# Kernel optimization log

Measured on AMD Instinct MI355X. Metric: run time of the kernel, lower is better.

The kernel has to match this reference:

```python
import jax, jax.numpy as jnp
import numpy as np

# dims: B batch, T timesteps, V nodes, D in-features, C channels, d pos-emb dim,
# TS = t_size (spatio-temporal window), P prediction steps, L layers (=4, fixed by GLU(C*4))
B, T, V, D, C, d, TS, P, L = 4, 12, 512, 1, 64, 8, 3, 12, 4
BETA = TS - 1


def setup_inputs() -> dict:
    key = jax.random.key(0)
    ks = jax.random.split(key, 30)
    n = lambda i, shape, s=1.0: jax.random.normal(ks[i], shape, dtype=jnp.float32) * s
    return dict(
        x=n(0, (B, T, V, D)),
        sape=n(1, (V, d)),
        tape=n(2, (B, T, 1, d)),
        srpe=n(3, (V, V, d)),
        trpe=n(4, (TS, 1, d)),
        zeros_x=jnp.zeros((B, BETA, V, C), jnp.float32),
        zeros_tape=jnp.zeros((B, BETA, 1, d), jnp.float32),
        range_mask=(jax.random.uniform(ks[5], (B, V, TS * V)) < 0.5).astype(jnp.float32),
        Wi=n(6, (D, C), D ** -0.5), bi=n(7, (C,), 0.02),
        gc_mu=n(8, (L, 6, d)), gc_sig=n(9, (L, 6, d), 0.5),
        Wg=n(10, (L, C, 2 * C), C ** -0.5), bg=n(11, (L, 2 * C), 0.02),
        Wsp=n(12, (L, d, 2 * C), d ** -0.5), Wtp=n(13, (L, d, 2 * C), d ** -0.5),
        fs_w=n(14, (L, C, C, T), (C * T) ** -0.5), fs_b=n(15, (L, C), 0.02),
        glu1_w=n(16, (L, 2 * C, C), C ** -0.5), glu1_b=n(17, (L, 2 * C), 0.02),
        gout_w=n(18, (8 * C, 4 * C), (4 * C) ** -0.5), gout_b=n(19, (8 * C,), 0.02),
        out_w=n(20, (P, 4 * C), (4 * C) ** -0.5), out_b=n(21, (P,), 0.02),
    )


def _glu_cv(w, b, y):
    # 1x1-conv GLU over channel dim of y: (B, Cin, V) -> (B, Cin, V)
    z = jnp.einsum('oc,bcv->bov', w, y) + b[None, :, None]
    zl, zr = jnp.split(z, 2, axis=1)
    return zl * jax.nn.sigmoid(zr)


def _forward(x, sape, tape, srpe, trpe, Wi, bi, gc_mu, gc_sig, Wg, bg, Wsp, Wtp,
             fs_w, fs_b, glu1_w, glu1_b, gout_w, gout_b, out_w, out_b,
             zeros_x, zeros_tape, range_mask):
    b_, t_ = x.shape[0], x.shape[1]
    v_ = sape.shape[0]
    ts = trpe.shape[0]
    widx = jnp.arange(t_)[:, None] + jnp.arange(ts)  # (T, t_size) sliding-window indices
    h = x @ Wi + bi                                   # InputLayer: B,T,V,C
    tape_pad = jnp.concatenate([zeros_tape, tape], axis=1)  # B,T+beta,1,d
    skips = []
    for l in range(gc_mu.shape[0]):
        mu, sig = gc_mu[l], gc_sig[l]
        gc = lambda emb, i: jnp.sum(-0.5 * (emb - mu[i]) ** 2 * sig[i] ** 2, axis=-1)
        # STPRI: Gaussian position-aware relation inference
        base = gc(sape, 0)[:, None] + gc(sape, 1)[None, :] + gc(srpe, 4)        # (V_i, V_j)
        per_t = gc(tape, 2)[:, :, 0][:, :, None] \
              + gc(tape_pad, 3)[:, :, 0][:, widx] \
              + gc(trpe, 5)[:, 0]                                               # B,T,t_size
        S = jnp.exp(per_t[:, :, :, None, None] + base)                          # B,T,k,i,j (<=1, safe)
        S = S.transpose(0, 1, 4, 2, 3).reshape(b_, t_, v_, ts * v_)             # B,T,j,(k*V+i)
        S = S * range_mask[:, None]                                             # masked relations
        # STPGConv: masked graph conv over the t_size*V window + gating
        x_pad = jnp.concatenate([zeros_x, h], axis=1)                           # B,T+beta,V,C
        xw = x_pad[:, widx].reshape(b_, t_, ts * v_, -1)                        # B,T,t_size*V,C
        g = jnp.einsum('btjm,btmc->btjc', S, xw) @ Wg[l] + bg[l]                # B,T,V,2C
        g = g + sape @ Wsp[l] + tape @ Wtp[l]                                   # +SE(V,2C) +TE(B,T,1,2C)
        gl, gr = jnp.split(g, 2, axis=-1)
        h = gl * jax.nn.sigmoid(gr)                                             # B,T,V,C
        # GFS: conv over time (kernel (1,T)) + GLU -> B,C,V
        y = jnp.einsum('bcvt,oct->bov', h.transpose(0, 3, 2, 1), fs_w[l]) + fs_b[l][None, :, None]
        skips.append(_glu_cv(glu1_w[l], glu1_b[l], y))
    s = _glu_cv(gout_w, gout_b, jnp.concatenate(skips, axis=1))                  # B,4C,V
    return jnp.einsum('oc,bcv->bov', out_w, s) + out_b[None, :, None]            # B,P,V


def reference(x, sape, tape, srpe, trpe, zeros_x, zeros_tape, range_mask, Wi, bi,
              gc_mu, gc_sig, Wg, bg, Wsp, Wtp, fs_w, fs_b, glu1_w, glu1_b,
              gout_w, gout_b, out_w, out_b):
    return _forward(x, sape, tape, srpe, trpe, Wi, bi, gc_mu, gc_sig, Wg, bg, Wsp, Wtp,
                    fs_w, fs_b, glu1_w, glu1_b, gout_w, gout_b, out_w, out_b,
                    zeros_x, zeros_tape, range_mask)
```

## Files before the change

kernel.cpp:

```cpp
#include <hip/hip_runtime.h>
#include <math.h>


typedef unsigned short u16;
typedef __attribute__((ext_vector_type(8))) short short8;
typedef __attribute__((ext_vector_type(4))) float f32x4;
typedef __attribute__((ext_vector_type(8))) unsigned short u16x8;
typedef __attribute__((ext_vector_type(4))) unsigned short u16x4;

#define MFMA16(a, b, c) __builtin_amdgcn_mfma_f32_16x16x32_bf16((a), (b), (c), 0, 0, 0)

__device__ __forceinline__ float b2f(u16 u) {
  union { unsigned int i; float f; } x; x.i = ((unsigned int)u) << 16; return x.f;
}
__device__ __forceinline__ u16 f2b(float f) {
  union { float f; unsigned int i; } x; x.f = f;
  unsigned int r = x.i + 0x7FFFu + ((x.i >> 16) & 1u);
  return (u16)(r >> 16);
}
__device__ __forceinline__ void ld8f(const float* __restrict__ p, float* f) {
  f32x4 a = *(const f32x4*)p;
  f32x4 b = *(const f32x4*)(p + 4);
  #pragma unroll
  for (int i = 0; i < 4; ++i) { f[i] = a[i]; f[4 + i] = b[i]; }
}
__device__ __forceinline__ float gcf(const float* e, const float* __restrict__ mu,
                                     const float* __restrict__ sg) {
  float s = 0.f;
  #pragma unroll
  for (int i = 0; i < 8; ++i) {
    float dm = e[i] - mu[i];
    s += dm * dm * sg[i] * sg[i];
  }
  return -0.5f * s;
}
__device__ __forceinline__ float sigm(float v) { return 1.0f / (1.0f + expf(-v)); }

__global__ __launch_bounds__(256) void prep_kernel(
    const float* __restrict__ x, const float* __restrict__ sape,
    const float* __restrict__ tape, const float* __restrict__ srpe,
    const float* __restrict__ trpe, const float* __restrict__ Wi,
    const float* __restrict__ bi, const float* __restrict__ gmu,
    const float* __restrict__ gsg, const float* __restrict__ Wg,
    const float* __restrict__ bg, const float* __restrict__ Wsp,
    const float* __restrict__ Wtp, const float* __restrict__ fsw,
    const float* __restrict__ mask,
    const float* __restrict__ g1w, const float* __restrict__ gw,
    const float* __restrict__ ow,
    u16* __restrict__ hT0, u16* __restrict__ Abf,
    float* __restrict__ spb, float* __restrict__ tpb,
    u16* __restrict__ fswT, u16* __restrict__ WgT, float* __restrict__ ev,
    u16* __restrict__ g1wB, u16* __restrict__ gwB, u16* __restrict__ owB) {
  const int tid = threadIdx.x;
  int bid = blockIdx.x;

  if (bid < 768) {
    int gid = bid * 256 + tid;
    int i8 = gid & 63, c = (gid >> 6) & 63, bt = gid >> 12;
    float xv[8];
    ld8f(&x[bt * 512 + i8 * 8], xv);
    float wic = Wi[c], bic = bi[c];
    u16x8 hv;
    #pragma unroll
    for (int ii = 0; ii < 8; ++ii) hv[ii] = f2b(xv[ii] * wic + bic);
    *(u16x8*)&hT0[gid * 8] = hv;
    return;
  }
  bid -= 768;
  if (bid < 1024) {
    int gid = bid * 256 + tid;
    int i = gid & 511, j = gid >> 9;
    float fi[8], fj[8], fr[8];
    ld8f(sape + i * 8, fi);
    ld8f(sape + j * 8, fj);
    ld8f(srpe + ((size_t)i * 512 + j) * 8, fr);
    u16 eb[4];
    #pragma unroll
    for (int l = 0; l < 4; ++l) {
      const float* mub = gmu + l * 48;
      const float* sgb = gsg + l * 48;
      float s = gcf(fi, mub + 0, sgb + 0)
              + gcf(fj, mub + 8, sgb + 8)
              + gcf(fr, mub + 32, sgb + 32);
      eb[l] = f2b(expf(s));
    }
    #pragma unroll
    for (int b = 0; b < 4; ++b)
      #pragma unroll
      for (int k = 0; k < 3; ++k) {
        float mv = mask[((size_t)(b * 512 + j)) * 1536 + k * 512 + i];
        u16 m = (mv != 0.f) ? (u16)0xFFFFu : (u16)0;
        #pragma unroll
        for (int l = 0; l < 4; ++l)
          Abf[((size_t)((l * 4 + b) * 512 + j)) * 1536 + k * 512 + i] = eb[l] & m;
      }
    return;
  }
  bid -= 1024;
  if (bid < 1024) {
    int gid = bid * 256 + tid;
    int o = gid & 127, j = (gid >> 7) & 511, l = gid >> 16;
    float a = 0.f;
    #pragma unroll
    for (int dd = 0; dd < 8; ++dd)
      a += sape[j * 8 + dd] * Wsp[(l * 8 + dd) * 128 + o];
    spb[gid] = a;
    return;
  }
  bid -= 1024;
  if (bid < 96) {
    int gid = bid * 256 + tid;
    int o = gid & 127, bt = (gid >> 7) % 48, l = gid / 6144;
    float a = bg[l * 128 + o];
    #pragma unroll
    for (int dd = 0; dd < 8; ++dd)
      a += tape[bt * 8 + dd] * Wtp[(l * 8 + dd) * 128 + o];
    tpb[gid] = a;
    return;
  }
  bid -= 96;
  if (bid < 768) {
    int gid = bid * 256 + tid;
    int kidx = gid % 768, rest = gid / 768;
    int o = rest & 63, l = rest >> 6;
    int c = kidx & 63, tt = kidx >> 6;
    fswT[gid] = f2b(fsw[((l * 64 + o) * 64 + c) * 12 + tt]);
    return;
  }
  bid -= 768;
  if (bid < 128) {
    int gid = bid * 256 + tid;
    int c = gid & 63, o = (gid >> 6) & 127, l = gid >> 13;
    WgT[gid] = f2b(Wg[(l * 64 + c) * 128 + o]);
    return;
  }
  bid -= 128;
  if (bid < 3) {
    int gid = bid * 256 + tid;
    if (gid < 576) {
      int k = gid % 3, t = (gid / 3) % 12, b = (gid / 36) % 4, l = gid / 144;
      const float* mub = gmu + l * 48;
      const float* sgb = gsg + l * 48;
      float e2[8], e3[8], e5[8];
      ld8f(tape + (b * 12 + t) * 8, e2);
      int tp = t + k - 2;
      if (tp >= 0) ld8f(tape + (b * 12 + tp) * 8, e3);
      else {
        #pragma unroll
        for (int ii = 0; ii < 8; ++ii) e3[ii] = 0.f;
      }
      ld8f(trpe + k * 8, e5);
      float s = gcf(e2, mub + 16, sgb + 16)
              + gcf(e3, mub + 24, sgb + 24)
              + gcf(e5, mub + 40, sgb + 40);
      ev[gid] = expf(s);
    }
    return;
  }
  bid -= 3;
  if (bid < 128) {
    int gid = bid * 256 + tid;
    g1wB[gid] = f2b(g1w[gid]);
    return;
  }
  bid -= 128;
  if (bid < 512) {
    int gid = bid * 256 + tid;
    gwB[gid] = f2b(gw[gid]);
    return;
  }
  bid -= 512;
  {
    int gid = bid * 256 + tid;
    if (gid < 3072) owB[gid] = f2b(ow[gid]);
  }
}

__global__ __launch_bounds__(256) void agg_kernel(
    const u16* __restrict__ Abfl, const u16* __restrict__ hT,
    u16* __restrict__ G) {
  __shared__ u16 As[128][72];
  __shared__ u16 Bs[128][72];
  const int tid = threadIdx.x, wid = tid >> 6, lane = tid & 63;
  const int l16 = lane & 15, quad = lane >> 4;
  const int bid = blockIdx.x;
  const int nt = bid % 6;
  const int mt = (bid / 6) & 3;
  const int k  = (bid / 24) % 3;
  const int b  = bid / 72;
  const int wm = wid >> 1, wn = wid & 1;

  const u16* Arow0 = Abfl + ((size_t)(b * 512 + mt * 128)) * 1536 + k * 512;
  f32x4 acc[4][4] = {};

  for (int it = 0; it < 8; ++it) {
    const int i0 = it * 64;
    #pragma unroll
    for (int s = 0; s < 4; ++s) {
      int idx = s * 256 + tid;
      int r = idx >> 3, ch = (idx & 7) * 8;
      *(u16x8*)&As[r][ch] = *(const u16x8*)&Arow0[(size_t)r * 1536 + i0 + ch];
      int tp = nt * 2 + (r >> 6), c = r & 63;
      *(u16x8*)&Bs[r][ch] =
          *(const u16x8*)&hT[((size_t)((b * 12 + tp) * 64 + c)) * 512 + i0 + ch];
    }
    __syncthreads();
    #pragma unroll
    for (int ks = 0; ks < 2; ++ks) {
      short8 af[4], bf[4];
      #pragma unroll
      for (int mb = 0; mb < 4; ++mb)
        af[mb] = *(const short8*)&As[wm * 64 + mb * 16 + l16][ks * 32 + quad * 8];
      #pragma unroll
      for (int nb = 0; nb < 4; ++nb)
        bf[nb] = *(const short8*)&Bs[wn * 64 + nb * 16 + l16][ks * 32 + quad * 8];
      #pragma unroll
      for (int mb = 0; mb < 4; ++mb)
        #pragma unroll
        for (int nb = 0; nb < 4; ++nb)
          acc[mb][nb] = MFMA16(af[mb], bf[nb], acc[mb][nb]);
    }
    __syncthreads();
  }

  u16* Gp = G + ((size_t)((b * 3 + k) * 512 + mt * 128)) * 768 + nt * 128;
  #pragma unroll
  for (int mb = 0; mb < 4; ++mb)
    #pragma unroll
    for (int nb = 0; nb < 4; ++nb) {
      int n = wn * 64 + nb * 16 + l16;
      #pragma unroll
      for (int r = 0; r < 4; ++r) {
        int m = wm * 64 + mb * 16 + quad * 4 + r;
        Gp[(size_t)m * 768 + n] = f2b(acc[mb][nb][r]);
      }
    }
}

__global__ __launch_bounds__(256) void combine_kernel(
    const u16* __restrict__ G, const float* __restrict__ evl,
    const u16* __restrict__ WgTl, const float* __restrict__ spbl,
    const float* __restrict__ tpbl, const u16* __restrict__ fswTl,
    u16* __restrict__ hTout, float* __restrict__ yptl) {
  __shared__ u16 aggL[128][72];
  __shared__ u16 hL[128][72];
  const int tid = threadIdx.x, wid = tid >> 6, lane = tid & 63;
  const int l16 = lane & 15, quad = lane >> 4;
  const int bid = blockIdx.x;
  const int mt = bid & 3;
  const int bt = bid >> 2;
  const int b = bt / 12, t = bt - b * 12;

  {
    int j = tid >> 1;
    int c0 = (tid & 1) * 32;
    float accv[32];
    #pragma unroll
    for (int ii = 0; ii < 32; ++ii) accv[ii] = 0.f;
    #pragma unroll
    for (int k = 0; k < 3; ++k) {
      int tp = t + k - 2;
      if (tp < 0) continue;
      float ek = evl[bt * 3 + k];
      const u16* gp = &G[((size_t)((b * 3 + k) * 512 + mt * 128 + j)) * 768 + tp * 64 + c0];
      #pragma unroll
      for (int s = 0; s < 4; ++s) {
        u16x8 gv = *(const u16x8*)&gp[s * 8];
        #pragma unroll
        for (int ii = 0; ii < 8; ++ii) accv[s * 8 + ii] += b2f(gv[ii]) * ek;
      }
    }
    #pragma unroll
    for (int s = 0; s < 4; ++s) {
      u16x8 ov;
      #pragma unroll
      for (int ii = 0; ii < 8; ++ii) ov[ii] = f2b(accv[s * 8 + ii]);
      *(u16x8*)&aggL[j][c0 + s * 8] = ov;
    }
  }
  __syncthreads();

  f32x4 acc2[8][2] = {};
  #pragma unroll
  for (int ks = 0; ks < 2; ++ks) {
    short8 bf[2];
    #pragma unroll
    for (int nb = 0; nb < 2; ++nb)
      bf[nb] = *(const short8*)&aggL[wid * 32 + nb * 16 + l16][ks * 32 + quad * 8];
    #pragma unroll
    for (int mb = 0; mb < 8; ++mb) {
      short8 a = *(const short8*)&WgTl[(mb * 16 + l16) * 64 + ks * 32 + quad * 8];
      acc2[mb][0] = MFMA16(a, bf[0], acc2[mb][0]);
      acc2[mb][1] = MFMA16(a, bf[1], acc2[mb][1]);
    }
  }

  #pragma unroll
  for (int mb = 0; mb < 4; ++mb) {
    int ob = mb * 16 + quad * 4;
    #pragma unroll
    for (int nb = 0; nb < 2; ++nb) {
      int jl = wid * 32 + nb * 16 + l16;
      int jg = mt * 128 + jl;
      f32x4 spl = *(const f32x4*)&spbl[jg * 128 + ob];
      f32x4 spr = *(const f32x4*)&spbl[jg * 128 + 64 + ob];
      f32x4 tpl = *(const f32x4*)&tpbl[bt * 128 + ob];
      f32x4 tpr = *(const f32x4*)&tpbl[bt * 128 + 64 + ob];
      #pragma unroll
      for (int r = 0; r < 4; ++r) {
        float vl = acc2[mb][nb][r] + spl[r] + tpl[r];
        float vr = acc2[mb + 4][nb][r] + spr[r] + tpr[r];
        u16 hb = f2b(vl * sigm(vr));
        hTout[((size_t)((b * 12 + t) * 64 + ob + r)) * 512 + jg] = hb;
        hL[jl][ob + r] = hb;
      }
    }
  }
  __syncthreads();

  f32x4 accY[4][2] = {};
  #pragma unroll
  for (int ks = 0; ks < 2; ++ks) {
    short8 bfv[2];
    #pragma unroll
    for (int nb = 0; nb < 2; ++nb)
      bfv[nb] = *(const short8*)&hL[wid * 32 + nb * 16 + l16][ks * 32 + quad * 8];
    #pragma unroll
    for (int mb = 0; mb < 4; ++mb) {
      short8 a = *(const short8*)&fswTl[(mb * 16 + l16) * 768 + t * 64 + ks * 32 + quad * 8];
      accY[mb][0] = MFMA16(a, bfv[0], accY[mb][0]);
      accY[mb][1] = MFMA16(a, bfv[1], accY[mb][1]);
    }
  }
  #pragma unroll
  for (int mb = 0; mb < 4; ++mb)
    #pragma unroll
    for (int nb = 0; nb < 2; ++nb) {
      int j = mt * 128 + wid * 32 + nb * 16 + l16;
      #pragma unroll
      for (int r = 0; r < 4; ++r) {
        int o = mb * 16 + quad * 4 + r;
        yptl[((size_t)(bt * 64 + o)) * 512 + j] = accY[mb][nb][r];
      }
    }
}

__global__ __launch_bounds__(256) void reduce_kernel(
    const float* __restrict__ ypt, const float* __restrict__ fsb,
    u16* __restrict__ yB) {
  int gid = blockIdx.x * 256 + threadIdx.x;
  int j4 = gid & 127, o = (gid >> 7) & 63, b = (gid >> 13) & 3, l = gid >> 15;
  const float* base = &ypt[(size_t)l * 1572864 +
                           ((size_t)((b * 12) * 64 + o)) * 512 + j4 * 4];
  float fb = fsb[l * 64 + o];
  f32x4 s = {fb, fb, fb, fb};
  #pragma unroll
  for (int t = 0; t < 12; ++t) s += *(const f32x4*)&base[(size_t)t * 32768];
  u16x4 pk;
  #pragma unroll
  for (int ii = 0; ii < 4; ++ii) pk[ii] = f2b(s[ii]);
  *(u16x4*)&yB[((size_t)((l * 4 + b) * 64 + o)) * 512 + j4 * 4] = pk;
}

__global__ __launch_bounds__(256) void final_kernel(
    const u16* __restrict__ yB,
    const u16* __restrict__ g1wB, const float* __restrict__ g1b,
    const u16* __restrict__ gwB, const float* __restrict__ gb,
    const u16* __restrict__ owB, const float* __restrict__ obv,
    float* __restrict__ out) {
  __shared__ u16 yL[64][72];
  __shared__ float zL[128][72];
  __shared__ u16 cL[64][264];
  __shared__ u16 sT[64][264];
  const int tid = threadIdx.x, wid = tid >> 6, lane = tid & 63;
  const int l16 = lane & 15, quad = lane >> 4;
  const int b = blockIdx.x >> 3;
  const int v0 = (blockIdx.x & 7) * 64;

  for (int l = 0; l < 4; ++l) {
    {
      int o = tid & 63, sv = tid >> 6;
      const u16* src = &yB[((size_t)((l * 4 + b) * 64 + o)) * 512 + v0 + sv * 16];
      u16x8 p0 = *(const u16x8*)&src[0];
      u16x8 p1 = *(const u16x8*)&src[8];
      #pragma unroll
      for (int ii = 0; ii < 8; ++ii) {
        yL[sv * 16 + ii][o] = p0[ii];
        yL[sv * 16 + 8 + ii][o] = p1[ii];
      }
    }
    __syncthreads();
    f32x4 a1[2][4] = {};
    #pragma unroll
    for (int ks = 0; ks < 2; ++ks) {
      short8 bfv[4];
      #pragma unroll
      for (int nb = 0; nb < 4; ++nb)
        bfv[nb] = *(const short8*)&yL[nb * 16 + l16][ks * 32 + quad * 8];
      #pragma unroll
      for (int mb = 0; mb < 2; ++mb) {
        short8 a = *(const short8*)&g1wB[l * 8192 + (wid * 32 + mb * 16 + l16) * 64 +
                                         ks * 32 + quad * 8];
        #pragma unroll
        for (int nb = 0; nb < 4; ++nb) a1[mb][nb] = MFMA16(a, bfv[nb], a1[mb][nb]);
      }
    }
    #pragma unroll
    for (int mb = 0; mb < 2; ++mb)
      #pragma unroll
      for (int nb = 0; nb < 4; ++nb)
        #pragma unroll
        for (int r = 0; r < 4; ++r)
          zL[wid * 32 + mb * 16 + quad * 4 + r][nb * 16 + l16] = a1[mb][nb][r];
    __syncthreads();
    {
      int o = tid >> 2, vv0 = (tid & 3) * 16;
      float bl = g1b[l * 128 + o], br = g1b[l * 128 + 64 + o];
      #pragma unroll
      for (int ii = 0; ii < 16; ++ii) {
        float zl = zL[o][vv0 + ii] + bl;
        float zr = zL[o + 64][vv0 + ii] + br;
        cL[vv0 + ii][l * 64 + o] = f2b(zl * sigm(zr));
      }
    }
    __syncthreads();
  }

  f32x4 acc[8][4] = {};
  #pragma unroll
  for (int ks = 0; ks < 8; ++ks) {
    short8 bf[4];
    #pragma unroll
    for (int nb = 0; nb < 4; ++nb)
      bf[nb] = *(const short8*)&cL[nb * 16 + l16][ks * 32 + quad * 8];
    #pragma unroll
    for (int mb = 0; mb < 8; ++mb) {
      int og = (mb < 4 ? wid * 64 + mb * 16 : 256 + wid * 64 + (mb - 4) * 16) + l16;
      short8 a = *(const short8*)&gwB[og * 256 + ks * 32 + quad * 8];
      #pragma unroll
      for (int nb = 0; nb < 4; ++nb) acc[mb][nb] = MFMA16(a, bf[nb], acc[mb][nb]);
    }
  }
  #pragma unroll
  for (int mb = 0; mb < 4; ++mb)
    #pragma unroll
    for (int nb = 0; nb < 4; ++nb) {
      int vloc = nb * 16 + l16;
      int cc0 = wid * 64 + mb * 16 + quad * 4;
      u16x4 pk;
      #pragma unroll
      for (int r = 0; r < 4; ++r) {
        float zl = acc[mb][nb][r] + gb[cc0 + r];
        float zr = acc[mb + 4][nb][r] + gb[256 + cc0 + r];
        pk[r] = f2b(zl * sigm(zr));
      }
      *(u16x4*)&sT[vloc][cc0] = pk;
    }
  __syncthreads();

  f32x4 acc3 = {};
  #pragma unroll
  for (int ks = 0; ks < 8; ++ks) {
    short8 a;
    if (l16 < 12) a = *(const short8*)&owB[l16 * 256 + ks * 32 + quad * 8];
    else {
      #pragma unroll
      for (int ii = 0; ii < 8; ++ii) a[ii] = 0;
    }
    short8 bf = *(const short8*)&sT[wid * 16 + l16][ks * 32 + quad * 8];
    acc3 = MFMA16(a, bf, acc3);
  }
  #pragma unroll
  for (int r = 0; r < 4; ++r) {
    int p = quad * 4 + r;
    if (p < 12)
      out[(b * 12 + p) * 512 + v0 + wid * 16 + l16] = acc3[r] + obv[p];
  }
}

extern "C" void kernel_launch(void* const* d_in, const int* in_sizes, int n_in,
                              void* d_out, int out_size, void* d_ws, size_t ws_size,
                              hipStream_t stream) {
  const float* x    = (const float*)d_in[0];
  const float* sape = (const float*)d_in[1];
  const float* tape = (const float*)d_in[2];
  const float* srpe = (const float*)d_in[3];
  const float* trpe = (const float*)d_in[4];
  const float* mask = (const float*)d_in[7];
  const float* Wi   = (const float*)d_in[8];
  const float* bi   = (const float*)d_in[9];
  const float* gmu  = (const float*)d_in[10];
  const float* gsg  = (const float*)d_in[11];
  const float* Wg   = (const float*)d_in[12];
  const float* bg   = (const float*)d_in[13];
  const float* Wsp  = (const float*)d_in[14];
  const float* Wtp  = (const float*)d_in[15];
  const float* fsw  = (const float*)d_in[16];
  const float* fsb  = (const float*)d_in[17];
  const float* g1w  = (const float*)d_in[18];
  const float* g1b  = (const float*)d_in[19];
  const float* gow  = (const float*)d_in[20];
  const float* gob  = (const float*)d_in[21];
  const float* ow   = (const float*)d_in[22];
  const float* obv  = (const float*)d_in[23];

  char* w = (char*)d_ws;
  u16*   hT_a = (u16*)(w + 0);
  u16*   hT_b = (u16*)(w + 3145728);
  u16*   Abf  = (u16*)(w + 6291456);
  u16*   G    = (u16*)(w + 31457280);
  u16*   fswT = (u16*)(w + 40894464);
  u16*   WgT  = (u16*)(w + 41287680);
  u16*   g1wB = (u16*)(w + 41353216);
  u16*   gwB  = (u16*)(w + 41418752);
  u16*   owB  = (u16*)(w + 41680896);
  float* spb  = (float*)(w + 41689088);
  float* tpb  = (float*)(w + 42737664);
  float* ev   = (float*)(w + 42835968);
  float* ypt  = (float*)(w + 42852352);
  u16*   yB   = (u16*)(w + 68018176);

  prep_kernel<<<4463, 256, 0, stream>>>(x, sape, tape, srpe, trpe, Wi, bi, gmu, gsg,
                                        Wg, bg, Wsp, Wtp, fsw, mask, g1w, gow, ow,
                                        hT_a, Abf, spb, tpb, fswT, WgT, ev,
                                        g1wB, gwB, owB);
  u16* hin = hT_a;
  u16* hout = hT_b;
  for (int l = 0; l < 4; ++l) {
    agg_kernel<<<288, 256, 0, stream>>>(Abf + (size_t)l * 3145728, hin, G);
    combine_kernel<<<192, 256, 0, stream>>>(G, ev + l * 144, WgT + l * 8192,
                                            spb + l * 65536, tpb + l * 6144,
                                            fswT + l * 49152, hout,
                                            ypt + (size_t)l * 1572864);
    u16* tmp = hin; hin = hout; hout = tmp;
  }
  reduce_kernel<<<512, 256, 0, stream>>>(ypt, fsb, yB);
  final_kernel<<<32, 256, 0, stream>>>(yB, g1wB, g1b, gwB, gob, owB, obv,
                                       (float*)d_out);
}
```

Baseline: 266.1 us.

## Fuse aggregation GEMM with combine/GLU/time-conv into a single per-layer kernel

Merges agg_kernel and combine_kernel into one layer_kernel. Each block computes the three window-offset aggregations for two timesteps, mixes them with the edge weights in registers, and then runs the Wg GEMM, GLU and fs-conv partial products. This removes the bf16 G intermediate round trip and one launch per layer. The fs partial sums are also pre-reduced over timestep pairs, which halves the ypt buffer that reduce_kernel reads. In exchange each block holds more accumulators (3x2x4 tiles), uses a smaller M tile, and skips work for negative timesteps, which leaves the load across blocks uneven.

```diff
diff --git a/kernel.cpp b/kernel.cpp
--- a/kernel.cpp
+++ b/kernel.cpp
@@ -176,190 +176,160 @@
   }
 }
 
-__global__ __launch_bounds__(256) void agg_kernel(
-    const u16* __restrict__ Abfl, const u16* __restrict__ hT,
-    u16* __restrict__ G) {
-  __shared__ u16 As[128][72];
+__global__ __launch_bounds__(256) void layer_kernel(
+    const u16* __restrict__ Abfl, const u16* __restrict__ hTin,
+    const float* __restrict__ evl, const u16* __restrict__ WgTl,
+    const float* __restrict__ spbl, const float* __restrict__ tpbl,
+    const u16* __restrict__ fswTl, u16* __restrict__ hTout,
+    float* __restrict__ ypnl) {
+  __shared__ u16 As[64][72];
   __shared__ u16 Bs[128][72];
+  __shared__ u16 Cs[2][64][72];
+  __shared__ u16 hL[64][72];
   const int tid = threadIdx.x, wid = tid >> 6, lane = tid & 63;
   const int l16 = lane & 15, quad = lane >> 4;
+  const int wm = wid >> 1, wn = wid & 1;
   const int bid = blockIdx.x;
   const int nt = bid % 6;
-  const int mt = (bid / 6) & 3;
-  const int k  = (bid / 24) % 3;
-  const int b  = bid / 72;
-  const int wm = wid >> 1, wn = wid & 1;
-
-  const u16* Arow0 = Abfl + ((size_t)(b * 512 + mt * 128)) * 1536 + k * 512;
-  f32x4 acc[4][4] = {};
-
-  for (int it = 0; it < 8; ++it) {
-    const int i0 = it * 64;
-    #pragma unroll
-    for (int s = 0; s < 4; ++s) {
-      int idx = s * 256 + tid;
-      int r = idx >> 3, ch = (idx & 7) * 8;
-      *(u16x8*)&As[r][ch] = *(const u16x8*)&Arow0[(size_t)r * 1536 + i0 + ch];
-      int tp = nt * 2 + (r >> 6), c = r & 63;
-      *(u16x8*)&Bs[r][ch] =
-          *(const u16x8*)&hT[((size_t)((b * 12 + tp) * 64 + c)) * 512 + i0 + ch];
+  const int mt = (bid / 6) & 7;
+  const int b  = bid / 48;
+
+  const int r0 = tid >> 3, ch0 = (tid & 7) * 8;
+  f32x4 acc[3][2][4] = {};
+
+  for (int k = 0; k < 3; ++k) {
+    const int tp0 = 2 * nt + k - 2;
+    if (tp0 + 1 < 0) continue;
+    for (int it = 0; it < 8; ++it) {
+      const int i0 = it * 64;
+      #pragma unroll
+      for (int s = 0; s < 2; ++s) {
+        int r = r0 + s * 32;
+        *(u16x8*)&As[r][ch0] =
+            *(const u16x8*)&Abfl[(size_t)(b * 512 + mt * 64 + r) * 1536 + k * 512 + i0 + ch0];
+      }
+      #pragma unroll
+      for (int s = 0; s < 4; ++s) {
+        int r = r0 + s * 32;
+        int tsel = r >> 6, c = r & 63;
+        int tp = tp0 + tsel;
+        u16x8 v;
+        if (tp >= 0)
+          v = *(const u16x8*)&hTin[((size_t)((b * 12 + tp) * 64 + c)) * 512 + i0 + ch0];
+        else {
+          #pragma unroll
+          for (int ii = 0; ii < 8; ++ii) v[ii] = 0;
+        }
+        *(u16x8*)&Bs[r][ch0] = v;
+      }
+      __syncthreads();
+      #pragma unroll
+      for (int ks = 0; ks < 2; ++ks) {
+        short8 af[2], bf[4];
+        #pragma unroll
+        for (int mb = 0; mb < 2; ++mb)
+          af[mb] = *(const short8*)&As[wm * 32 + mb * 16 + l16][ks * 32 + quad * 8];
+        #pragma unroll
+        for (int nb = 0; nb < 4; ++nb)
+          bf[nb] = *(const short8*)&Bs[wn * 64 + nb * 16 + l16][ks * 32 + quad * 8];
+        #pragma unroll
+        for (int mb = 0; mb < 2; ++mb)
+          #pragma unroll
+          for (int nb = 0; nb < 4; ++nb)
+            acc[k][mb][nb] = MFMA16(af[mb], bf[nb], acc[k][mb][nb]);
+      }
+      __syncthreads();
+    }
+  }
+
+  {
+    const int t_w = 2 * nt + wn;
+    const float e0 = evl[(b * 12 + t_w) * 3 + 0];
+    const float e1 = evl[(b * 12 + t_w) * 3 + 1];
+    const float e2 = evl[(b * 12 + t_w) * 3 + 2];
+    #pragma unroll
+    for (int mb = 0; mb < 2; ++mb)
+      #pragma unroll
+      for (int nb = 0; nb < 4; ++nb)
+        #pragma unroll
+        for (int r = 0; r < 4; ++r) {
+          float cv = e0 * acc[0][mb][nb][r] + e1 * acc[1][mb][nb][r] +
+                     e2 * acc[2][mb][nb][r];
+          Cs[wn][wm * 32 + mb * 16 + quad * 4 + r][nb * 16 + l16] = f2b(cv);
+        }
+  }
+  __syncthreads();
+
+  f32x4 accY[4] = {};
+  for (int tsel = 0; tsel < 2; ++tsel) {
+    const int t = 2 * nt + tsel, bt = b * 12 + t;
+    f32x4 a2[2][4] = {};
+    #pragma unroll
+    for (int ks = 0; ks < 2; ++ks) {
+      short8 bf[4];
+      #pragma unroll
+      for (int nb = 0; nb < 4; ++nb)
+        bf[nb] = *(const short8*)&Cs[tsel][nb * 16 + l16][ks * 32 + quad * 8];
+      #pragma unroll
+      for (int mb = 0; mb < 2; ++mb) {
+        short8 a = *(const short8*)&WgTl[(mb * 64 + wid * 16 + l16) * 64 +
+                                         ks * 32 + quad * 8];
+        #pragma unroll
+        for (int nb = 0; nb < 4; ++nb) a2[mb][nb] = MFMA16(a, bf[nb], a2[mb][nb]);
+      }
+    }
+    #pragma unroll
+    for (int nb = 0; nb < 4; ++nb) {
+      int jg = mt * 64 + nb * 16 + l16;
+      #pragma unroll
+      for (int r = 0; r < 4; ++r) {
+        int o = wid * 16 + quad * 4 + r;
+        float vl = a2[0][nb][r] + spbl[jg * 128 + o] + tpbl[bt * 128 + o];
+        float vr = a2[1][nb][r] + spbl[jg * 128 + 64 + o] + tpbl[bt * 128 + 64 + o];
+        u16 hb = f2b(vl * sigm(vr));
+        hTout[((size_t)(bt * 64 + o)) * 512 + jg] = hb;
+        hL[nb * 16 + l16][o] = hb;
+      }
     }
     __syncthreads();
     #pragma unroll
     for (int ks = 0; ks < 2; ++ks) {
-      short8 af[4], bf[4];
-      #pragma unroll
-      for (int mb = 0; mb < 4; ++mb)
-        af[mb] = *(const short8*)&As[wm * 64 + mb * 16 + l16][ks * 32 + quad * 8];
-      #pragma unroll
-      for (int nb = 0; nb < 4; ++nb)
-        bf[nb] = *(const short8*)&Bs[wn * 64 + nb * 16 + l16][ks * 32 + quad * 8];
-      #pragma unroll
-      for (int mb = 0; mb < 4; ++mb)
-        #pragma unroll
-        for (int nb = 0; nb < 4; ++nb)
-          acc[mb][nb] = MFMA16(af[mb], bf[nb], acc[mb][nb]);
+      short8 a = *(const short8*)&fswTl[(wid * 16 + l16) * 768 + t * 64 +
+                                        ks * 32 + quad * 8];
+      #pragma unroll
+      for (int nb = 0; nb < 4; ++nb) {
+        short8 bf = *(const short8*)&hL[nb * 16 + l16][ks * 32 + quad * 8];
+        accY[nb] = MFMA16(a, bf, accY[nb]);
+      }
     }
     __syncthreads();
   }
-
-  u16* Gp = G + ((size_t)((b * 3 + k) * 512 + mt * 128)) * 768 + nt * 128;
-  #pragma unroll
-  for (int mb = 0; mb < 4; ++mb)
-    #pragma unroll
-    for (int nb = 0; nb < 4; ++nb) {
-      int n = wn * 64 + nb * 16 + l16;
-      #pragma unroll
-      for (int r = 0; r < 4; ++r) {
-        int m = wm * 64 + mb * 16 + quad * 4 + r;
-        Gp[(size_t)m * 768 + n] = f2b(acc[mb][nb][r]);
-      }
-    }
-}
-
-__global__ __launch_bounds__(256) void combine_kernel(
-    const u16* __restrict__ G, const float* __restrict__ evl,
-    const u16* __restrict__ WgTl, const float* __restrict__ spbl,
-    const float* __restrict__ tpbl, const u16* __restrict__ fswTl,
-    u16* __restrict__ hTout, float* __restrict__ yptl) {
-  __shared__ u16 aggL[128][72];
-  __shared__ u16 hL[128][72];
-  const int tid = threadIdx.x, wid = tid >> 6, lane = tid & 63;
-  const int l16 = lane & 15, quad = lane >> 4;
-  const int bid = blockIdx.x;
-  const int mt = bid & 3;
-  const int bt = bid >> 2;
-  const int b = bt / 12, t = bt - b * 12;
-
-  {
-    int j = tid >> 1;
-    int c0 = (tid & 1) * 32;
-    float accv[32];
-    #pragma unroll
-    for (int ii = 0; ii < 32; ++ii) accv[ii] = 0.f;
-    #pragma unroll
-    for (int k = 0; k < 3; ++k) {
-      int tp = t + k - 2;
-      if (tp < 0) continue;
-      float ek = evl[bt * 3 + k];
-      const u16* gp = &G[((size_t)((b * 3 + k) * 512 + mt * 128 + j)) * 768 + tp * 64 + c0];
-      #pragma unroll
-      for (int s = 0; s < 4; ++s) {
-        u16x8 gv = *(const u16x8*)&gp[s * 8];
-        #pragma unroll
-        for (int ii = 0; ii < 8; ++ii) accv[s * 8 + ii] += b2f(gv[ii]) * ek;
-      }
-    }
-    #pragma unroll
-    for (int s = 0; s < 4; ++s) {
-      u16x8 ov;
-      #pragma unroll
-      for (int ii = 0; ii < 8; ++ii) ov[ii] = f2b(accv[s * 8 + ii]);
-      *(u16x8*)&aggL[j][c0 + s * 8] = ov;
-    }
-  }
-  __syncthreads();
-
-  f32x4 acc2[8][2] = {};
-  #pragma unroll
-  for (int ks = 0; ks < 2; ++ks) {
-    short8 bf[2];
-    #pragma unroll
-    for (int nb = 0; nb < 2; ++nb)
-      bf[nb] = *(const short8*)&aggL[wid * 32 + nb * 16 + l16][ks * 32 + quad * 8];
-    #pragma unroll
-    for (int mb = 0; mb < 8; ++mb) {
-      short8 a = *(const short8*)&WgTl[(mb * 16 + l16) * 64 + ks * 32 + quad * 8];
-      acc2[mb][0] = MFMA16(a, bf[0], acc2[mb][0]);
-      acc2[mb][1] = MFMA16(a, bf[1], acc2[mb][1]);
-    }
-  }
-
-  #pragma unroll
-  for (int mb = 0; mb < 4; ++mb) {
-    int ob = mb * 16 + quad * 4;
-    #pragma unroll
-    for (int nb = 0; nb < 2; ++nb) {
-      int jl = wid * 32 + nb * 16 + l16;
-      int jg = mt * 128 + jl;
-      f32x4 spl = *(const f32x4*)&spbl[jg * 128 + ob];
-      f32x4 spr = *(const f32x4*)&spbl[jg * 128 + 64 + ob];
-      f32x4 tpl = *(const f32x4*)&tpbl[bt * 128 + ob];
-      f32x4 tpr = *(const f32x4*)&tpbl[bt * 128 + 64 + ob];
-      #pragma unroll
-      for (int r = 0; r < 4; ++r) {
-        float vl = acc2[mb][nb][r] + spl[r] + tpl[r];
-        float vr = acc2[mb + 4][nb][r] + spr[r] + tpr[r];
-        u16 hb = f2b(vl * sigm(vr));
-        hTout[((size_t)((b * 12 + t) * 64 + ob + r)) * 512 + jg] = hb;
-        hL[jl][ob + r] = hb;
-      }
-    }
-  }
-  __syncthreads();
-
-  f32x4 accY[4][2] = {};
-  #pragma unroll
-  for (int ks = 0; ks < 2; ++ks) {
-    short8 bfv[2];
-    #pragma unroll
-    for (int nb = 0; nb < 2; ++nb)
-      bfv[nb] = *(const short8*)&hL[wid * 32 + nb * 16 + l16][ks * 32 + quad * 8];
-    #pragma unroll
-    for (int mb = 0; mb < 4; ++mb) {
-      short8 a = *(const short8*)&fswTl[(mb * 16 + l16) * 768 + t * 64 + ks * 32 + quad * 8];
-      accY[mb][0] = MFMA16(a, bfv[0], accY[mb][0]);
-      accY[mb][1] = MFMA16(a, bfv[1], accY[mb][1]);
-    }
-  }
-  #pragma unroll
-  for (int mb = 0; mb < 4; ++mb)
-    #pragma unroll
-    for (int nb = 0; nb < 2; ++nb) {
-      int j = mt * 128 + wid * 32 + nb * 16 + l16;
-      #pragma unroll
-      for (int r = 0; r < 4; ++r) {
-        int o = mb * 16 + quad * 4 + r;
-        yptl[((size_t)(bt * 64 + o)) * 512 + j] = accY[mb][nb][r];
-      }
-    }
+  #pragma unroll
+  for (int nb = 0; nb < 4; ++nb) {
+    int jg = mt * 64 + nb * 16 + l16;
+    #pragma unroll
+    for (int r = 0; r < 4; ++r) {
+      int o2 = wid * 16 + quad * 4 + r;
+      ypnl[((size_t)(b * 6 + nt)) * 32768 + o2 * 512 + jg] = accY[nb][r];
+    }
+  }
 }
 
 __global__ __launch_bounds__(256) void reduce_kernel(
-    const float* __restrict__ ypt, const float* __restrict__ fsb,
+    const float* __restrict__ ypn, const float* __restrict__ fsb,
     u16* __restrict__ yB) {
   int gid = blockIdx.x * 256 + threadIdx.x;
-  int j4 = gid & 127, o = (gid >> 7) & 63, b = (gid >> 13) & 3, l = gid >> 15;
-  const float* base = &ypt[(size_t)l * 1572864 +
-                           ((size_t)((b * 12) * 64 + o)) * 512 + j4 * 4];
+  int v4 = gid & 127, o = (gid >> 7) & 63, b = (gid >> 13) & 3, l = gid >> 15;
+  const float* base = &ypn[(size_t)l * 786432 + ((size_t)(b * 6)) * 32768 +
+                           o * 512 + v4 * 4];
   float fb = fsb[l * 64 + o];
   f32x4 s = {fb, fb, fb, fb};
   #pragma unroll
-  for (int t = 0; t < 12; ++t) s += *(const f32x4*)&base[(size_t)t * 32768];
+  for (int nt = 0; nt < 6; ++nt) s += *(const f32x4*)&base[(size_t)nt * 32768];
   u16x4 pk;
   #pragma unroll
   for (int ii = 0; ii < 4; ++ii) pk[ii] = f2b(s[ii]);
-  *(u16x4*)&yB[((size_t)((l * 4 + b) * 64 + o)) * 512 + j4 * 4] = pk;
+  *(u16x4*)&yB[((size_t)((l * 4 + b) * 64 + o)) * 512 + v4 * 4] = pk;
 }
 
 __global__ __launch_bounds__(256) void final_kernel(
@@ -508,17 +478,16 @@
   u16*   hT_a = (u16*)(w + 0);
   u16*   hT_b = (u16*)(w + 3145728);
   u16*   Abf  = (u16*)(w + 6291456);
-  u16*   G    = (u16*)(w + 31457280);
-  u16*   fswT = (u16*)(w + 40894464);
-  u16*   WgT  = (u16*)(w + 41287680);
-  u16*   g1wB = (u16*)(w + 41353216);
-  u16*   gwB  = (u16*)(w + 41418752);
-  u16*   owB  = (u16*)(w + 41680896);
-  float* spb  = (float*)(w + 41689088);
-  float* tpb  = (float*)(w + 42737664);
-  float* ev   = (float*)(w + 42835968);
-  float* ypt  = (float*)(w + 42852352);
-  u16*   yB   = (u16*)(w + 68018176);
+  u16*   fswT = (u16*)(w + 31457280);
+  u16*   WgT  = (u16*)(w + 31850496);
+  u16*   g1wB = (u16*)(w + 31916032);
+  u16*   gwB  = (u16*)(w + 31981568);
+  u16*   owB  = (u16*)(w + 32243712);
+  float* spb  = (float*)(w + 32251904);
+  float* tpb  = (float*)(w + 33300480);
+  float* ev   = (float*)(w + 33398784);
+  float* ypn  = (float*)(w + 33415168);
+  u16*   yB   = (u16*)(w + 45998080);
 
   prep_kernel<<<4463, 256, 0, stream>>>(x, sape, tape, srpe, trpe, Wi, bi, gmu, gsg,
                                         Wg, bg, Wsp, Wtp, fsw, mask, g1w, gow, ow,
@@ -527,14 +496,14 @@
   u16* hin = hT_a;
   u16* hout = hT_b;
   for (int l = 0; l < 4; ++l) {
-    agg_kernel<<<288, 256, 0, stream>>>(Abf + (size_t)l * 3145728, hin, G);
-    combine_kernel<<<192, 256, 0, stream>>>(G, ev + l * 144, WgT + l * 8192,
-                                            spb + l * 65536, tpb + l * 6144,
-                                            fswT + l * 49152, hout,
-                                            ypt + (size_t)l * 1572864);
+    layer_kernel<<<192, 256, 0, stream>>>(Abf + (size_t)l * 3145728, hin,
+                                          ev + l * 144, WgT + l * 8192,
+                                          spb + l * 65536, tpb + l * 6144,
+                                          fswT + l * 49152, hout,
+                                          ypn + (size_t)l * 786432);
     u16* tmp = hin; hin = hout; hout = tmp;
   }
-  reduce_kernel<<<512, 256, 0, stream>>>(ypt, fsb, yB);
+  reduce_kernel<<<512, 256, 0, stream>>>(ypn, fsb, yB);
   final_kernel<<<32, 256, 0, stream>>>(yB, g1wB, g1b, gwB, gob, owB, obv,
                                        (float*)d_out);
 }
```

After: 347.7 us. +30.7%, slower.

## Split final tail kernel into three kernels to raise parallelism

Applied to the files above, without the earlier changes.

Replaces the single 32-block final kernel, which ran the per-layer GLU, the output GLU and the head serially, with three kernels. The per-layer GLU writes a concatenated bf16 buffer from 64 blocks, the 256x512 gout GLU runs over 256 blocks, and the head projection reads from global memory. The aim is to fill more compute units on a tail that was starved of parallelism. The cost is two extra launches and extra global round trips for the intermediate buffers.

```diff
diff --git a/kernel.cpp b/kernel.cpp
--- a/kernel.cpp
+++ b/kernel.cpp
@@ -362,103 +362,120 @@
   *(u16x4*)&yB[((size_t)((l * 4 + b) * 64 + o)) * 512 + j4 * 4] = pk;
 }
 
-__global__ __launch_bounds__(256) void final_kernel(
-    const u16* __restrict__ yB,
-    const u16* __restrict__ g1wB, const float* __restrict__ g1b,
-    const u16* __restrict__ gwB, const float* __restrict__ gb,
-    const u16* __restrict__ owB, const float* __restrict__ obv,
-    float* __restrict__ out) {
-  __shared__ u16 yL[64][72];
-  __shared__ float zL[128][72];
+__global__ __launch_bounds__(256) void glu1cat_kernel(
+    const u16* __restrict__ yB, const u16* __restrict__ g1wB,
+    const float* __restrict__ g1b, u16* __restrict__ catB) {
+  __shared__ u16 yL[128][72];
+  const int tid = threadIdx.x, wid = tid >> 6, lane = tid & 63;
+  const int l16 = lane & 15, quad = lane >> 4;
+  const int l = blockIdx.x >> 4;
+  const int b = (blockIdx.x >> 2) & 3;
+  const int v0 = (blockIdx.x & 3) * 128;
+
+  {
+    int o = tid & 63, sv = tid >> 6;
+    const u16* src = &yB[((size_t)((l * 4 + b) * 64 + o)) * 512 + v0 + sv * 32];
+    u16x8 p0 = *(const u16x8*)&src[0];
+    u16x8 p1 = *(const u16x8*)&src[8];
+    u16x8 p2 = *(const u16x8*)&src[16];
+    u16x8 p3 = *(const u16x8*)&src[24];
+    #pragma unroll
+    for (int ii = 0; ii < 8; ++ii) {
+      yL[sv * 32 + ii][o] = p0[ii];
+      yL[sv * 32 + 8 + ii][o] = p1[ii];
+      yL[sv * 32 + 16 + ii][o] = p2[ii];
+      yL[sv * 32 + 24 + ii][o] = p3[ii];
+    }
+  }
+  __syncthreads();
+
+  f32x4 acc[2][8] = {};
+  #pragma unroll
+  for (int ks = 0; ks < 2; ++ks) {
+    short8 a0 = *(const short8*)&g1wB[l * 8192 + (wid * 16 + l16) * 64 +
+                                      ks * 32 + quad * 8];
+    short8 a1 = *(const short8*)&g1wB[l * 8192 + (64 + wid * 16 + l16) * 64 +
+                                      ks * 32 + quad * 8];
+    #pragma unroll
+    for (int nb = 0; nb < 8; ++nb) {
+      short8 bf = *(const short8*)&yL[nb * 16 + l16][ks * 32 + quad * 8];
+      acc[0][nb] = MFMA16(a0, bf, acc[0][nb]);
+      acc[1][nb] = MFMA16(a1, bf, acc[1][nb]);
+    }
+  }
+  #pragma unroll
+  for (int nb = 0; nb < 8; ++nb) {
+    int v = v0 + nb * 16 + l16;
+    int oc = wid * 16 + quad * 4;
+    u16x4 pk;
+    #pragma unroll
+    for (int r = 0; r < 4; ++r) {
+      float zl = acc[0][nb][r] + g1b[l * 128 + oc + r];
+      float zr = acc[1][nb][r] + g1b[l * 128 + 64 + oc + r];
+      pk[r] = f2b(zl * sigm(zr));
+    }
+    *(u16x4*)&catB[((size_t)(b * 512 + v)) * 256 + l * 64 + oc] = pk;
+  }
+}
+
+__global__ __launch_bounds__(256) void gout_kernel(
+    const u16* __restrict__ catB, const u16* __restrict__ gwB,
+    const float* __restrict__ gb, u16* __restrict__ sB) {
   __shared__ u16 cL[64][264];
-  __shared__ u16 sT[64][264];
+  const int tid = threadIdx.x, wid = tid >> 6, lane = tid & 63;
+  const int l16 = lane & 15, quad = lane >> 4;
+  const int wm = wid >> 1, wn = wid & 1;
+  const int b = blockIdx.x >> 6;
+  const int v0 = ((blockIdx.x >> 3) & 7) * 64;
+  const int cc0 = (blockIdx.x & 7) * 32;
+
+  {
+    int v = tid >> 2, seg = (tid & 3) * 64;
+    const u16* src = &catB[((size_t)(b * 512 + v0 + v)) * 256 + seg];
+    #pragma unroll
+    for (int s = 0; s < 8; ++s)
+      *(u16x8*)&cL[v][seg + s * 8] = *(const u16x8*)&src[s * 8];
+  }
+  __syncthreads();
+
+  f32x4 acc[2][2] = {};
+  #pragma unroll
+  for (int ks = 0; ks < 8; ++ks) {
+    short8 aL = *(const short8*)&gwB[(cc0 + wm * 16 + l16) * 256 +
+                                     ks * 32 + quad * 8];
+    short8 aH = *(const short8*)&gwB[(256 + cc0 + wm * 16 + l16) * 256 +
+                                     ks * 32 + quad * 8];
+    #pragma unroll
+    for (int nb = 0; nb < 2; ++nb) {
+      short8 bf = *(const short8*)&cL[wn * 32 + nb * 16 + l16][ks * 32 + quad * 8];
+      acc[0][nb] = MFMA16(aL, bf, acc[0][nb]);
+      acc[1][nb] = MFMA16(aH, bf, acc[1][nb]);
+    }
+  }
+  #pragma unroll
+  for (int nb = 0; nb < 2; ++nb) {
+    int v = v0 + wn * 32 + nb * 16 + l16;
+    int cc = cc0 + wm * 16 + quad * 4;
+    u16x4 pk;
+    #pragma unroll
+    for (int r = 0; r < 4; ++r) {
+      float zl = acc[0][nb][r] + gb[cc + r];
+      float zr = acc[1][nb][r] + gb[256 + cc + r];
+      pk[r] = f2b(zl * sigm(zr));
+    }
+    *(u16x4*)&sB[((size_t)(b * 512 + v)) * 256 + cc] = pk;
+  }
+}
+
+__global__ __launch_bounds__(256) void head_kernel(
+    const u16* __restrict__ sB, const u16* __restrict__ owB,
+    const float* __restrict__ obv, float* __restrict__ out) {
   const int tid = threadIdx.x, wid = tid >> 6, lane = tid & 63;
   const int l16 = lane & 15, quad = lane >> 4;
   const int b = blockIdx.x >> 3;
   const int v0 = (blockIdx.x & 7) * 64;
 
-  for (int l = 0; l < 4; ++l) {
-    {
-      int o = tid & 63, sv = tid >> 6;
-      const u16* src = &yB[((size_t)((l * 4 + b) * 64 + o)) * 512 + v0 + sv * 16];
-      u16x8 p0 = *(const u16x8*)&src[0];
-      u16x8 p1 = *(const u16x8*)&src[8];
-      #pragma unroll
-      for (int ii = 0; ii < 8; ++ii) {
-        yL[sv * 16 + ii][o] = p0[ii];
-        yL[sv * 16 + 8 + ii][o] = p1[ii];
-      }
-    }
-    __syncthreads();
-    f32x4 a1[2][4] = {};
-    #pragma unroll
-    for (int ks = 0; ks < 2; ++ks) {
-      short8 bfv[4];
-      #pragma unroll
-      for (int nb = 0; nb < 4; ++nb)
-        bfv[nb] = *(const short8*)&yL[nb * 16 + l16][ks * 32 + quad * 8];
-      #pragma unroll
-      for (int mb = 0; mb < 2; ++mb) {
-        short8 a = *(const short8*)&g1wB[l * 8192 + (wid * 32 + mb * 16 + l16) * 64 +
-                                         ks * 32 + quad * 8];
-        #pragma unroll
-        for (int nb = 0; nb < 4; ++nb) a1[mb][nb] = MFMA16(a, bfv[nb], a1[mb][nb]);
-      }
-    }
-    #pragma unroll
-    for (int mb = 0; mb < 2; ++mb)
-      #pragma unroll
-      for (int nb = 0; nb < 4; ++nb)
-        #pragma unroll
-        for (int r = 0; r < 4; ++r)
-          zL[wid * 32 + mb * 16 + quad * 4 + r][nb * 16 + l16] = a1[mb][nb][r];
-    __syncthreads();
-    {
-      int o = tid >> 2, vv0 = (tid & 3) * 16;
-      float bl = g1b[l * 128 + o], br = g1b[l * 128 + 64 + o];
-      #pragma unroll
-      for (int ii = 0; ii < 16; ++ii) {
-        float zl = zL[o][vv0 + ii] + bl;
-        float zr = zL[o + 64][vv0 + ii] + br;
-        cL[vv0 + ii][l * 64 + o] = f2b(zl * sigm(zr));
-      }
-    }
-    __syncthreads();
-  }
-
-  f32x4 acc[8][4] = {};
-  #pragma unroll
-  for (int ks = 0; ks < 8; ++ks) {
-    short8 bf[4];
-    #pragma unroll
-    for (int nb = 0; nb < 4; ++nb)
-      bf[nb] = *(const short8*)&cL[nb * 16 + l16][ks * 32 + quad * 8];
-    #pragma unroll
-    for (int mb = 0; mb < 8; ++mb) {
-      int og = (mb < 4 ? wid * 64 + mb * 16 : 256 + wid * 64 + (mb - 4) * 16) + l16;
-      short8 a = *(const short8*)&gwB[og * 256 + ks * 32 + quad * 8];
-      #pragma unroll
-      for (int nb = 0; nb < 4; ++nb) acc[mb][nb] = MFMA16(a, bf[nb], acc[mb][nb]);
-    }
-  }
-  #pragma unroll
-  for (int mb = 0; mb < 4; ++mb)
-    #pragma unroll
-    for (int nb = 0; nb < 4; ++nb) {
-      int vloc = nb * 16 + l16;
-      int cc0 = wid * 64 + mb * 16 + quad * 4;
-      u16x4 pk;
-      #pragma unroll
-      for (int r = 0; r < 4; ++r) {
-        float zl = acc[mb][nb][r] + gb[cc0 + r];
-        float zr = acc[mb + 4][nb][r] + gb[256 + cc0 + r];
-        pk[r] = f2b(zl * sigm(zr));
-      }
-      *(u16x4*)&sT[vloc][cc0] = pk;
-    }
-  __syncthreads();
-
-  f32x4 acc3 = {};
+  f32x4 acc = {};
   #pragma unroll
   for (int ks = 0; ks < 8; ++ks) {
     short8 a;
@@ -467,14 +484,15 @@
       #pragma unroll
       for (int ii = 0; ii < 8; ++ii) a[ii] = 0;
     }
-    short8 bf = *(const short8*)&sT[wid * 16 + l16][ks * 32 + quad * 8];
-    acc3 = MFMA16(a, bf, acc3);
+    short8 bf = *(const short8*)&sB[((size_t)(b * 512 + v0 + wid * 16 + l16)) * 256 +
+                                    ks * 32 + quad * 8];
+    acc = MFMA16(a, bf, acc);
   }
   #pragma unroll
   for (int r = 0; r < 4; ++r) {
     int p = quad * 4 + r;
     if (p < 12)
-      out[(b * 12 + p) * 512 + v0 + wid * 16 + l16] = acc3[r] + obv[p];
+      out[(b * 12 + p) * 512 + v0 + wid * 16 + l16] = acc[r] + obv[p];
   }
 }
 
@@ -519,6 +537,8 @@
   float* ev   = (float*)(w + 42835968);
   float* ypt  = (float*)(w + 42852352);
   u16*   yB   = (u16*)(w + 68018176);
+  u16*   catB = (u16*)(w + 70115328);
+  u16*   sB   = (u16*)(w + 71163904);
 
   prep_kernel<<<4463, 256, 0, stream>>>(x, sape, tape, srpe, trpe, Wi, bi, gmu, gsg,
                                         Wg, bg, Wsp, Wtp, fsw, mask, g1w, gow, ow,
@@ -535,6 +555,7 @@
     u16* tmp = hin; hin = hout; hout = tmp;
   }
   reduce_kernel<<<512, 256, 0, stream>>>(ypt, fsb, yB);
-  final_kernel<<<32, 256, 0, stream>>>(yB, g1wB, g1b, gwB, gob, owB, obv,
-                                       (float*)d_out);
-}
+  glu1cat_kernel<<<64, 256, 0, stream>>>(yB, g1wB, g1b, catB);
+  gout_kernel<<<256, 256, 0, stream>>>(catB, gwB, gob, sB);
+  head_kernel<<<32, 256, 0, stream>>>(sB, owB, obv, (float*)d_out);
+}
```

Result: faster. 250.3 us (-5.9%).
